# Performance work log

Hardware: AMD Instinct MI355X
Metric: run time of the kernel (lower is better)

## Reference

```python
import jax, jax.numpy as jnp
import numpy as np

B, CIN, D = 4096, 4, 8
EPS = 1e-5
NEG_SLOPE = 0.01


def _conv3d(x, w):
    # x: [B,C,D,H,W], w: [kD,kH,kW,Cin,Cout]
    return jax.lax.conv_general_dilated(
        x, w, window_strides=(1, 1, 1), padding='SAME',
        dimension_numbers=('NCDHW', 'DHWIO', 'NCDHW'))


def _bn(x, gamma, beta, mean, var):
    s = (1, -1) + (1,) * (x.ndim - 2)
    inv = gamma.reshape(s) / jnp.sqrt(var.reshape(s) + EPS)
    return (x - mean.reshape(s)) * inv + beta.reshape(s)


def _maxpool2(x):
    return jax.lax.reduce_window(x, -jnp.inf, jax.lax.max,
                                 (1, 1, 2, 2, 2), (1, 1, 2, 2, 2), 'VALID')


def setup_inputs() -> dict:
    key = jax.random.key(0)
    ks = jax.random.split(key, 16)
    mask = jax.random.randint(ks[0], (B, D, D, D), 0, 2).astype(bool)
    x = jax.random.normal(ks[1], (B, CIN, D, D, D), jnp.float32)
    x = x * mask[:, None].astype(jnp.float32)  # sparse tensor: zeros off active sites
    def he(k, shape, fan_in):
        return jax.random.normal(k, shape, jnp.float32) * (2.0 / fan_in) ** 0.5
    return {
        'x': x, 'mask': mask,
        'W1': he(ks[2], (3, 3, 3, CIN, 32), 27 * CIN),
        'g1': jnp.ones((32,)), 'b1': jnp.zeros((32,)),
        'm1': jax.random.normal(ks[3], (32,)) * 0.1,
        'v1': jax.random.uniform(ks[4], (32,), minval=0.5, maxval=1.5),
        'W2': he(ks[5], (3, 3, 3, 32, 64), 27 * 32),
        'g2': jnp.ones((64,)), 'b2': jnp.zeros((64,)),
        'm2': jax.random.normal(ks[6], (64,)) * 0.1,
        'v2': jax.random.uniform(ks[7], (64,), minval=0.5, maxval=1.5),
        'fcw1': he(ks[8], (128, 512), 512), 'fcb1': jnp.zeros((128,)),
        'fcw2': he(ks[9], (1, 128), 128), 'fcb2': jnp.zeros((1,)),
    }


def reference(x, mask, W1, g1, b1, m1, v1, W2, g2, b2, m2, v2, fcw1, fcb1, fcw2, fcb2):
    mf = mask.astype(x.dtype)[:, None]          # [B,1,8,8,8] active-site mask
    # SubMConv3d(CIN->32): conv restricted to active output sites
    h = _conv3d(x, W1) * mf
    h = jax.nn.relu(_bn(h, g1, b1, m1, v1) * mf)   # BN on active features only
    h = _maxpool2(h)                             # [B,32,4,4,4]
    mf2 = _maxpool2(mf)                          # active if any voxel in window active
    # SubMConv3d(32->64)
    h = _conv3d(h, W2) * mf2
    h = jax.nn.relu(_bn(h, g2, b2, m2, v2) * mf2)
    h = _maxpool2(h)                             # [B,64,2,2,2]
    h = h.reshape(h.shape[0], -1)                # [B,512]
    h = h @ fcw1.T + fcb1
    h = jnp.where(h >= 0, h, NEG_SLOPE * h)      # LeakyReLU
    # dropout: identity at inference
    return h @ fcw2.T + fcb2                     # [B,1]
```

## Files before the change

### kernel.cpp

```cpp
#include <hip/hip_runtime.h>
#include <hip/hip_bf16.h>

typedef unsigned short u16;
typedef unsigned int   u32;
typedef short bf16x8 __attribute__((ext_vector_type(8)));
typedef short bf16x4 __attribute__((ext_vector_type(4)));
typedef float f32x4  __attribute__((ext_vector_type(4)));

#define EPS 1e-5f

#define HBG_N   (4096 * 512)
#define W2B_OFF HBG_N
#define W1B_OFF (W2B_OFF + 55296)
#define FCW_OFF (W1B_OFF + 4096)

__device__ __forceinline__ u16 f2bf(float f) {
    __hip_bfloat16 h = __float2bfloat16(f);
    return *(const u16*)&h;
}

union BV { bf16x8 v; bf16x4 h[2]; };

__global__ __launch_bounds__(256) void prep_kernel(
        const float* __restrict__ W2, const float* __restrict__ W1,
        const float* __restrict__ fcw1, u16* __restrict__ ws) {
    int i = blockIdx.x * 256 + threadIdx.x;
    if (i < 55296) {
        int tap = i >> 11, rem = i & 2047;
        int co = rem >> 5, ci = rem & 31;
        ws[W2B_OFF + i] = f2bf(W2[(size_t)tap * 2048 + ci * 64 + co]);
    }
    if (i < 4096) {
        int j = i & 7, cout = (i >> 3) & 31, quad = (i >> 8) & 3, ks = i >> 10;
        int tap = ks * 8 + quad * 2 + (j >> 2), ci = j & 3;
        ws[W1B_OFF + i] = (tap < 27) ? f2bf(W1[tap * 128 + ci * 32 + cout]) : (u16)0;
    }
    if (i < 65536)
        ws[FCW_OFF + i] = f2bf(fcw1[i]);
}

__global__ __launch_bounds__(512) void conv_kernel(
        const float* __restrict__ x,    const u32*  __restrict__ mask,
        const float* __restrict__ g1,   const float* __restrict__ b1,
        const float* __restrict__ m1,   const float* __restrict__ v1,
        const float* __restrict__ g2,   const float* __restrict__ b2,
        const float* __restrict__ m2,   const float* __restrict__ v2,
        u16* __restrict__ ws) {

    const u16* w2b = ws + W2B_OFF;
    const u16* w1b = ws + W1B_OFF;

    __shared__ __align__(16) u16 xb[2][1000 * 4];
    __shared__ int   msk[2][512];
    __shared__ __align__(16) u16 act[2][216 * 40];
    __shared__ float mf2s[2][64];
    __shared__ float h2f[2][512];
    __shared__ float sc1s[32], sh1s[32], sc2s[64], sh2s[64];

    const int b2i = blockIdx.x * 2;
    const int t   = threadIdx.x;

    if (t < 32) {
        float sc = g1[t] / sqrtf(v1[t] + EPS);
        sc1s[t] = sc; sh1s[t] = b1[t] - m1[t] * sc;
    } else if (t < 96) {
        int c = t - 32;
        float sc = g2[c] / sqrtf(v2[c] + EPS);
        sc2s[c] = sc; sh2s[c] = b2[c] - m2[c] * sc;
    }
    {
        const uint4 z4 = make_uint4(0u, 0u, 0u, 0u);
        for (int i = t; i < 1000; i += 512) ((uint4*)xb)[i]  = z4;
        for (int i = t; i < 2160; i += 512) ((uint4*)act)[i] = z4;
    }
    __syncthreads();

    {
        #pragma unroll
        for (int rep = 0; rep < 2; ++rep) {
            const int sl = t + rep * 512;
            const int it = sl >> 9, s = sl & 511;
            const float* xp = x + (size_t)(b2i + it) * 2048;
            const u32*   mp = mask + (size_t)(b2i + it) * 512;
            float a0 = xp[s], a1 = xp[512 + s], a2 = xp[1024 + s], a3 = xp[1536 + s];
            int z = s >> 6, y = (s >> 3) & 7, xx = s & 7;
            int row = z * 100 + y * 10 + xx + 111;
            ((u32*)(xb[it]))[row * 2]     = (u32)f2bf(a0) | ((u32)f2bf(a1) << 16);
            ((u32*)(xb[it]))[row * 2 + 1] = (u32)f2bf(a2) | ((u32)f2bf(a3) << 16);
            msk[it][s] = (mp[s] != 0u);
        }
    }
    __syncthreads();

    const int lane = t & 63;
    const int n    = lane & 15;
    const int quad = lane >> 4;
    const int w8   = __builtin_amdgcn_readfirstlane(t >> 6);
    const int it   = w8 >> 2;
    const int w    = w8 & 3;
    const u16* xbI  = xb[it];
    const int* mskI = msk[it];
    u16* actI = act[it];

    {
        bf16x8 afr[4][2];
        #pragma unroll
        for (int ks = 0; ks < 4; ++ks)
            #pragma unroll
            for (int mt = 0; mt < 2; ++mt)
                afr[ks][mt] = *(const bf16x8*)(w1b +
                    (((ks * 4 + quad) * 32) + mt * 16 + n) * 8);

        int dA[8];
        #pragma unroll
        for (int q = 0; q < 8; ++q) {
            int tap = (q >> 1) * 8 + quad * 2 + (q & 1);
            int tc = (tap < 27) ? tap : 26;
            int kd = tc / 9, rr = tc - kd * 9, kh = rr / 3, kw = rr - kh * 3;
            dA[q] = (kd - 1) * 100 + (kh - 1) * 10 + (kw - 1);
        }

        const int py_ = n >> 2, px_ = n & 3;
        float pmax[8];
        #pragma unroll
        for (int j = 0; j < 8; ++j) pmax[j] = 0.f;
        int any = 0;

        #pragma unroll
        for (int i = 0; i < 8; ++i) {
            const int z  = 2 * w   + (i >> 2);
            const int y  = 2 * py_ + ((i >> 1) & 1);
            const int xx = 2 * px_ + (i & 1);
            const int sPad = z * 100 + y * 10 + xx + 111;

            f32x4 acc0 = (f32x4){0.f, 0.f, 0.f, 0.f};
            f32x4 acc1 = (f32x4){0.f, 0.f, 0.f, 0.f};

            #pragma unroll
            for (int ks = 0; ks < 4; ++ks) {
                BV bv;
                bv.h[0] = *(const bf16x4*)(xbI + (sPad + dA[ks * 2])     * 4);
                bv.h[1] = *(const bf16x4*)(xbI + (sPad + dA[ks * 2 + 1]) * 4);
                acc0 = __builtin_amdgcn_mfma_f32_16x16x32_bf16(afr[ks][0], bv.v, acc0, 0, 0, 0);
                acc1 = __builtin_amdgcn_mfma_f32_16x16x32_bf16(afr[ks][1], bv.v, acc1, 0, 0, 0);
            }

            const int mbit = mskI[z * 64 + y * 8 + xx];
            const float mk = mbit ? 1.f : 0.f;
            any |= mbit;
            #pragma unroll
            for (int r = 0; r < 4; ++r) {
                int c0 = quad * 4 + r, c1 = 16 + quad * 4 + r;
                pmax[r]     = fmaxf(pmax[r],     fmaxf(acc0[r] * sc1s[c0] + sh1s[c0], 0.f) * mk);
                pmax[4 + r] = fmaxf(pmax[4 + r], fmaxf(acc1[r] * sc1s[c1] + sh1s[c1], 0.f) * mk);
            }
        }

        const int prow = (w + 1) * 36 + (py_ + 1) * 6 + (px_ + 1);
        #pragma unroll
        for (int mt = 0; mt < 2; ++mt) {
            u32 lo = (u32)f2bf(pmax[mt * 4])     | ((u32)f2bf(pmax[mt * 4 + 1]) << 16);
            u32 hi = (u32)f2bf(pmax[mt * 4 + 2]) | ((u32)f2bf(pmax[mt * 4 + 3]) << 16);
            ((u32*)actI)[prow * 20 + mt * 8 + quad * 2]     = lo;
            ((u32*)actI)[prow * 20 + mt * 8 + quad * 2 + 1] = hi;
        }
        if (quad == 0) mf2s[it][w * 16 + n] = any ? 1.f : 0.f;
    }
    __syncthreads();

    {
        const int nPad = ((n >> 2) + 1) * 6 + (n & 3) + 1;

        f32x4 acc[4];
        #pragma unroll
        for (int g = 0; g < 4; ++g) acc[g] = (f32x4){0.f, 0.f, 0.f, 0.f};

        #pragma unroll
        for (int kh = 0; kh < 3; ++kh) {
            #pragma unroll
            for (int kw = 0; kw < 3; ++kw) {
                bf16x8 bz[4];
                #pragma unroll
                for (int s = 0; s < 4; ++s)
                    bz[s] = *(const bf16x8*)(actI +
                        (nPad + (s + 1) * 36 + (kh - 1) * 6 + (kw - 1)) * 40 + quad * 8);
                #pragma unroll
                for (int kd = 0; kd < 3; ++kd) {
                    const int tap = (kd * 3 + kh) * 3 + kw;
                    bf16x8 afrag = *(const bf16x8*)(w2b + tap * 2048 + (w * 16 + n) * 32 + quad * 8);
                    #pragma unroll
                    for (int g = 0; g < 4; ++g) {
                        const int gp = g + kd - 1;
                        if (gp < 0 || gp > 3) continue;
                        acc[g] = __builtin_amdgcn_mfma_f32_16x16x32_bf16(
                                     afrag, bz[gp], acc[g], 0, 0, 0);
                    }
                }
            }
        }

        #pragma unroll
        for (int r = 0; r < 4; ++r) {
            const int cout = w * 16 + quad * 4 + r;
            float p2g[4];
            #pragma unroll
            for (int g = 0; g < 4; ++g) {
                const int site = g * 16 + n;
                float val = fmaxf(acc[g][r] * sc2s[cout] + sh2s[cout], 0.f) * mf2s[it][site];
                float p1 = fmaxf(val, __shfl_xor(val, 1, 64));
                p2g[g]   = fmaxf(p1,  __shfl_xor(p1, 4, 64));
            }
            if ((n & 5) == 0) {
                const int py = (n >> 3) & 1, px = (n >> 1) & 1;
                h2f[it][cout * 8 + 0 * 4 + py * 2 + px] = fmaxf(p2g[0], p2g[1]);
                h2f[it][cout * 8 + 1 * 4 + py * 2 + px] = fmaxf(p2g[2], p2g[3]);
            }
        }
    }
    __syncthreads();

    {
        const int pit = t >> 8, j = t & 255;
        u32 pk = (u32)f2bf(h2f[pit][2 * j]) | ((u32)f2bf(h2f[pit][2 * j + 1]) << 16);
        ((u32*)ws)[(size_t)(b2i + pit) * 256 + j] = pk;
    }
}

__global__ __launch_bounds__(256) void fc_kernel(
        const u16* __restrict__ ws,
        const float* __restrict__ fcb1, const float* __restrict__ fcw2,
        const float* __restrict__ fcb2, float* __restrict__ out) {

    const u16* hbg   = ws;
    const u16* fcw1b = ws + FCW_OFF;

    __shared__ __align__(16) u16 abuf[16 * 520];
    __shared__ float fcpart[16][4];

    const int t = threadIdx.x;
    const int item0 = blockIdx.x * 16;

    {
        const int it = t >> 4, part = t & 15;
        const uint4* src = (const uint4*)(hbg + (size_t)(item0 + it) * 512 + part * 32);
        uint4* dst = (uint4*)(abuf + it * 520 + part * 32);
        #pragma unroll
        for (int c = 0; c < 4; ++c) dst[c] = src[c];
    }
    __syncthreads();

    const int lane = t & 63;
    const int n    = lane & 15;
    const int quad = lane >> 4;
    const int w    = __builtin_amdgcn_readfirstlane(t >> 6);
    const int jbase = w * 32;

    float fb1[2], fw2[2];
    #pragma unroll
    for (int nt = 0; nt < 2; ++nt) {
        fb1[nt] = fcb1[jbase + nt * 16 + n];
        fw2[nt] = fcw2[jbase + nt * 16 + n];
    }

    f32x4 acc[2];
    acc[0] = (f32x4){0.f, 0.f, 0.f, 0.f};
    acc[1] = (f32x4){0.f, 0.f, 0.f, 0.f};

    #pragma unroll
    for (int ks = 0; ks < 16; ++ks) {
        bf16x8 afr = *(const bf16x8*)(abuf + n * 520 + ks * 32 + quad * 8);
        #pragma unroll
        for (int nt = 0; nt < 2; ++nt) {
            bf16x8 bfr = *(const bf16x8*)(fcw1b + (size_t)(jbase + nt * 16 + n) * 512 + ks * 32 + quad * 8);
            acc[nt] = __builtin_amdgcn_mfma_f32_16x16x32_bf16(afr, bfr, acc[nt], 0, 0, 0);
        }
    }

    #pragma unroll
    for (int r = 0; r < 4; ++r) {
        float s = 0.f;
        #pragma unroll
        for (int nt = 0; nt < 2; ++nt) {
            float y = acc[nt][r] + fb1[nt];
            y = (y >= 0.f) ? y : 0.01f * y;
            s += y * fw2[nt];
        }
        s += __shfl_xor(s, 1, 64);
        s += __shfl_xor(s, 2, 64);
        s += __shfl_xor(s, 4, 64);
        s += __shfl_xor(s, 8, 64);
        if (n == 0) fcpart[quad * 4 + r][w] = s;
    }
    __syncthreads();
    if (t < 16)
        out[item0 + t] = fcpart[t][0] + fcpart[t][1] + fcpart[t][2] + fcpart[t][3] + fcb2[0];
}

extern "C" void kernel_launch(void* const* d_in, const int* in_sizes, int n_in,
                              void* d_out, int out_size, void* d_ws, size_t ws_size,
                              hipStream_t stream) {
    const float* x    = (const float*)d_in[0];
    const u32*   mask = (const u32*)d_in[1];
    const float* W1   = (const float*)d_in[2];
    const float* g1   = (const float*)d_in[3];
    const float* b1   = (const float*)d_in[4];
    const float* m1   = (const float*)d_in[5];
    const float* v1   = (const float*)d_in[6];
    const float* W2   = (const float*)d_in[7];
    const float* g2   = (const float*)d_in[8];
    const float* b2   = (const float*)d_in[9];
    const float* m2   = (const float*)d_in[10];
    const float* v2   = (const float*)d_in[11];
    const float* fcw1 = (const float*)d_in[12];
    const float* fcb1 = (const float*)d_in[13];
    const float* fcw2 = (const float*)d_in[14];
    const float* fcb2 = (const float*)d_in[15];
    u16*   ws  = (u16*)d_ws;
    float* out = (float*)d_out;

    prep_kernel<<<256, 256, 0, stream>>>(W2, W1, fcw1, ws);
    conv_kernel<<<2048, 512, 0, stream>>>(
        x, mask, g1, b1, m1, v1, g2, b2, m2, v2, ws);
    fc_kernel<<<256, 256, 0, stream>>>(ws, fcb1, fcw2, fcb2, out);
}
```

Baseline: 158.8 us.

## Fuse FC head into conv kernel, dropping intermediate global round trip

```diff
diff --git a/kernel.cpp b/kernel.cpp
--- a/kernel.cpp
+++ b/kernel.cpp
@@ -45,16 +45,20 @@
         const float* __restrict__ m1,   const float* __restrict__ v1,
         const float* __restrict__ g2,   const float* __restrict__ b2,
         const float* __restrict__ m2,   const float* __restrict__ v2,
+        const float* __restrict__ fcb1, const float* __restrict__ fcw2,
+        const float* __restrict__ fcb2, float* __restrict__ out,
         u16* __restrict__ ws) {
 
     const u16* w2b = ws + W2B_OFF;
     const u16* w1b = ws + W1B_OFF;
+    const u16* fcw1b = ws + FCW_OFF;
 
     __shared__ __align__(16) u16 xb[2][1000 * 4];
     __shared__ int   msk[2][512];
     __shared__ __align__(16) u16 act[2][216 * 40];
     __shared__ float mf2s[2][64];
-    __shared__ float h2f[2][512];
+    __shared__ __align__(16) float h2f[2][512];
+    __shared__ float fcp[8][2];
     __shared__ float sc1s[32], sh1s[32], sc2s[64], sh2s[64];
 
     const int b2i = blockIdx.x * 2;
@@ -220,80 +224,38 @@
     __syncthreads();
 
     {
-        const int pit = t >> 8, j = t & 255;
-        u32 pk = (u32)f2bf(h2f[pit][2 * j]) | ((u32)f2bf(h2f[pit][2 * j + 1]) << 16);
-        ((u32*)ws)[(size_t)(b2i + pit) * 256 + j] = pk;
-    }
-}
-
-__global__ __launch_bounds__(256) void fc_kernel(
-        const u16* __restrict__ ws,
-        const float* __restrict__ fcb1, const float* __restrict__ fcw2,
-        const float* __restrict__ fcb2, float* __restrict__ out) {
-
-    const u16* hbg   = ws;
-    const u16* fcw1b = ws + FCW_OFF;
-
-    __shared__ __align__(16) u16 abuf[16 * 520];
-    __shared__ float fcpart[16][4];
-
-    const int t = threadIdx.x;
-    const int item0 = blockIdx.x * 16;
-
-    {
-        const int it = t >> 4, part = t & 15;
-        const uint4* src = (const uint4*)(hbg + (size_t)(item0 + it) * 512 + part * 32);
-        uint4* dst = (uint4*)(abuf + it * 520 + part * 32);
-        #pragma unroll
-        for (int c = 0; c < 4; ++c) dst[c] = src[c];
-    }
-    __syncthreads();
-
-    const int lane = t & 63;
-    const int n    = lane & 15;
-    const int quad = lane >> 4;
-    const int w    = __builtin_amdgcn_readfirstlane(t >> 6);
-    const int jbase = w * 32;
-
-    float fb1[2], fw2[2];
-    #pragma unroll
-    for (int nt = 0; nt < 2; ++nt) {
-        fb1[nt] = fcb1[jbase + nt * 16 + n];
-        fw2[nt] = fcw2[jbase + nt * 16 + n];
-    }
-
-    f32x4 acc[2];
-    acc[0] = (f32x4){0.f, 0.f, 0.f, 0.f};
-    acc[1] = (f32x4){0.f, 0.f, 0.f, 0.f};
-
-    #pragma unroll
-    for (int ks = 0; ks < 16; ++ks) {
-        bf16x8 afr = *(const bf16x8*)(abuf + n * 520 + ks * 32 + quad * 8);
-        #pragma unroll
-        for (int nt = 0; nt < 2; ++nt) {
-            bf16x8 bfr = *(const bf16x8*)(fcw1b + (size_t)(jbase + nt * 16 + n) * 512 + ks * 32 + quad * 8);
-            acc[nt] = __builtin_amdgcn_mfma_f32_16x16x32_bf16(afr, bfr, acc[nt], 0, 0, 0);
-        }
-    }
-
-    #pragma unroll
-    for (int r = 0; r < 4; ++r) {
-        float s = 0.f;
-        #pragma unroll
-        for (int nt = 0; nt < 2; ++nt) {
-            float y = acc[nt][r] + fb1[nt];
-            y = (y >= 0.f) ? y : 0.01f * y;
-            s += y * fw2[nt];
-        }
-        s += __shfl_xor(s, 1, 64);
-        s += __shfl_xor(s, 2, 64);
-        s += __shfl_xor(s, 4, 64);
-        s += __shfl_xor(s, 8, 64);
-        if (n == 0) fcpart[quad * 4 + r][w] = s;
-    }
-    __syncthreads();
-    if (t < 16)
-        out[item0 + t] = fcpart[t][0] + fcpart[t][1] + fcpart[t][2] + fcpart[t][3] + fcb2[0];
+        const int j = w8 * 16 + n;
+
+        f32x4 acc = (f32x4){0.f, 0.f, 0.f, 0.f};
+        #pragma unroll
+        for (int ks = 0; ks < 16; ++ks) {
+            bf16x8 afr = {0, 0, 0, 0, 0, 0, 0, 0};
+            if (n < 2) {
+                const float* hp = &h2f[n][ks * 32 + quad * 8];
+                #pragma unroll
+                for (int e = 0; e < 8; ++e) afr[e] = (short)f2bf(hp[e]);
+            }
+            bf16x8 bfr = *(const bf16x8*)(fcw1b + (size_t)j * 512 + ks * 32 + quad * 8);
+            acc = __builtin_amdgcn_mfma_f32_16x16x32_bf16(afr, bfr, acc, 0, 0, 0);
+        }
+
+        const float b1v = fcb1[j], w2v = fcw2[j];
+        float y0 = acc[0] + b1v; y0 = (y0 >= 0.f) ? y0 : 0.01f * y0;
+        float y1 = acc[1] + b1v; y1 = (y1 >= 0.f) ? y1 : 0.01f * y1;
+        float c0 = y0 * w2v, c1 = y1 * w2v;
+        c0 += __shfl_xor(c0, 1, 64); c1 += __shfl_xor(c1, 1, 64);
+        c0 += __shfl_xor(c0, 2, 64); c1 += __shfl_xor(c1, 2, 64);
+        c0 += __shfl_xor(c0, 4, 64); c1 += __shfl_xor(c1, 4, 64);
+        c0 += __shfl_xor(c0, 8, 64); c1 += __shfl_xor(c1, 8, 64);
+        if (lane == 0) { fcp[w8][0] = c0; fcp[w8][1] = c1; }
+    }
+    __syncthreads();
+    if (t < 2) {
+        float s = fcb2[0];
+        #pragma unroll
+        for (int v = 0; v < 8; ++v) s += fcp[v][t];
+        out[b2i + t] = s;
+    }
 }
 
 extern "C" void kernel_launch(void* const* d_in, const int* in_sizes, int n_in,
@@ -320,6 +282,6 @@
 
     prep_kernel<<<256, 256, 0, stream>>>(W2, W1, fcw1, ws);
     conv_kernel<<<2048, 512, 0, stream>>>(
-        x, mask, g1, b1, m1, v1, g2, b2, m2, v2, ws);
-    fc_kernel<<<256, 256, 0, stream>>>(ws, fcb1, fcw2, fcb2, out);
-}
+        x, mask, g1, b1, m1, v1, g2, b2, m2, v2,
+        fcb1, fcw2, fcb2, out, ws);
+}
```

After: 206.5 us. 1.3x slower.
